# Kernel optimization log

Measured on AMD Instinct MI355X. Metric: run time of the kernel, lower is better.

Reference implementation:

```python
import jax, jax.numpy as jnp
import numpy as np
import math

D_MODEL = 1024
NUM_HEADS = 16
D_HEAD = D_MODEL // NUM_HEADS
BATCH = 2
SEQ = 2048
ROPE_BASE = 10000.0


def get_rotary_embedding(seq_len, d_head):
    # standard RoPE tables: cos/sin of shape [seq_len, d_head]
    inv_freq = 1.0 / (ROPE_BASE ** (jnp.arange(0, d_head, 2, dtype=jnp.float32) / d_head))
    t = jnp.arange(seq_len, dtype=jnp.float32)
    freqs = jnp.outer(t, inv_freq)                      # [S, d_head/2]
    emb = jnp.concatenate([freqs, freqs], axis=-1)      # [S, d_head]
    return jnp.cos(emb), jnp.sin(emb)


def rotate_half(x):
    x1, x2 = jnp.split(x, 2, axis=-1)
    return jnp.concatenate([-x2, x1], axis=-1)


def apply_rotary_pos_emb(x, cos, sin):
    # x: [B, H, S, Dh]; cos/sin: [S, Dh] broadcast over B, H
    return x * cos[None, None, :, :] + rotate_half(x) * sin[None, None, :, :]


def setup_inputs() -> dict:
    key = jax.random.key(0)
    ks = jax.random.split(key, 9)
    s = 1.0 / math.sqrt(D_MODEL)
    inp = {
        "x":  jax.random.normal(ks[0], (BATCH, SEQ, D_MODEL), dtype=jnp.float32),
        "Wq": jax.random.uniform(ks[1], (D_MODEL, D_MODEL), jnp.float32, -s, s),
        "bq": jnp.zeros((D_MODEL,), jnp.float32),
        "Wk": jax.random.uniform(ks[2], (D_MODEL, D_MODEL), jnp.float32, -s, s),
        "bk": jnp.zeros((D_MODEL,), jnp.float32),
        "Wv": jax.random.uniform(ks[3], (D_MODEL, D_MODEL), jnp.float32, -s, s),
        "bv": jnp.zeros((D_MODEL,), jnp.float32),
        "Wo": jax.random.uniform(ks[4], (D_MODEL, D_MODEL), jnp.float32, -s, s),
        "bo": jnp.zeros((D_MODEL,), jnp.float32),
    }
    return inp


def reference(x, Wq, bq, Wk, bk, Wv, bv, Wo, bo) -> jnp.ndarray:
    B, S, _ = x.shape
    H, Dh = NUM_HEADS, D_HEAD

    def proj(W, b):
        y = jnp.einsum('bsd,ed->bse', x, W) + b          # nn.Linear: x @ W^T + b
        return y.reshape(B, S, H, Dh).transpose(0, 2, 1, 3)  # [B,H,S,Dh]

    Q = proj(Wq, bq)
    K = proj(Wk, bk)
    V = proj(Wv, bv)

    cos, sin = get_rotary_embedding(S, Dh)
    Q = apply_rotary_pos_emb(Q, cos, sin)
    K = apply_rotary_pos_emb(K, cos, sin)

    scores = jnp.einsum('bhqd,bhkd->bhqk', Q, K) / math.sqrt(Dh)  # [B,H,S,S]
    causal = jnp.tril(jnp.ones((S, S), dtype=bool))
    scores = jnp.where(causal[None, None, :, :], scores, -jnp.inf)
    attn = jax.nn.softmax(scores, axis=-1)
    # dropout is identity in eval / p=0
    context = jnp.einsum('bhqk,bhkd->bhqd', attn, V)               # [B,H,S,Dh]
    context = context.transpose(0, 2, 1, 3).reshape(B, S, H * Dh)
    return jnp.einsum('bsd,ed->bse', context, Wo) + bo
```

## Files before the change

kernel.cpp:

```cpp
#include <hip/hip_runtime.h>
#include <hip/hip_bf16.h>
#include <math.h>

typedef __attribute__((ext_vector_type(8))) short short8;
typedef __attribute__((ext_vector_type(8))) __bf16 bf16x8;
typedef __attribute__((ext_vector_type(4))) float f32x4;
typedef __attribute__((ext_vector_type(16))) float f32x16;

#define D_MODEL 1024
#define NUM_HEADS 16
#define D_HEAD 64
#define BATCH 2
#define SEQ 2048
#define BH (BATCH * NUM_HEADS)
#define MTOT (BATCH * SEQ)

__device__ inline f32x4 mfma16(short8 a, short8 b, f32x4 c) {
  return __builtin_amdgcn_mfma_f32_16x16x32_bf16(
      __builtin_bit_cast(bf16x8, a), __builtin_bit_cast(bf16x8, b), c, 0, 0, 0);
}

__device__ inline f32x16 mfma32(short8 a, short8 b, f32x16 c) {
  return __builtin_amdgcn_mfma_f32_32x32x16_bf16(
      __builtin_bit_cast(bf16x8, a), __builtin_bit_cast(bf16x8, b), c, 0, 0, 0);
}

__device__ inline unsigned short f2b(float f) {
  __hip_bfloat16 h = __float2bfloat16(f);
  return __builtin_bit_cast(unsigned short, h);
}

__device__ inline unsigned cvt_pk_bf16(float lo, float hi) {
  unsigned r;
  asm("v_cvt_pk_bf16_f32 %0, %1, %2" : "=v"(r) : "v"(lo), "v"(hi));
  return r;
}

__device__ inline float exp2_hw(float x) {
  float r;
  asm("v_exp_f32 %0, %1" : "=v"(r) : "v"(x));
  return r;
}

__device__ inline void permlane32_swap(unsigned& a, unsigned& b) {
  asm("v_permlane32_swap_b32 %0, %1" : "+v"(a), "+v"(b));
}

__device__ __forceinline__ void wait_barrier_vm0() {
  asm volatile("s_waitcnt vmcnt(0)\n\ts_barrier" ::: "memory");
}

#define GLOAD_LDS16(gaddr, laddr)                                              \
  __builtin_amdgcn_global_load_lds(                                            \
      (const __attribute__((address_space(1))) void*)(gaddr),                  \
      (__attribute__((address_space(3))) void*)(laddr), 16, 0, 0)

__global__ void cvt_f32_bf16(const float* __restrict__ in,
                             unsigned short* __restrict__ out, int n) {
  int i = (blockIdx.x * 256 + threadIdx.x) * 4;
  if (i >= n) return;
  float4 v = *(const float4*)(in + i);
  ushort4 o;
  o.x = f2b(v.x); o.y = f2b(v.y); o.z = f2b(v.z); o.w = f2b(v.w);
  *(ushort4*)(out + i) = o;
}

__global__ void cvt4_f32_bf16(const float* __restrict__ w0, const float* __restrict__ w1,
                              const float* __restrict__ w2, const float* __restrict__ w3,
                              unsigned short* __restrict__ o0, unsigned short* __restrict__ o1,
                              unsigned short* __restrict__ o2, unsigned short* __restrict__ o3,
                              int n) {
  const float* in; unsigned short* out;
  switch (blockIdx.y) {
    case 0: in = w0; out = o0; break;
    case 1: in = w1; out = o1; break;
    case 2: in = w2; out = o2; break;
    default: in = w3; out = o3; break;
  }
  int i = (blockIdx.x * 256 + threadIdx.x) * 4;
  if (i >= n) return;
  float4 v = *(const float4*)(in + i);
  ushort4 o;
  o.x = f2b(v.x); o.y = f2b(v.y); o.z = f2b(v.z); o.w = f2b(v.w);
  *(ushort4*)(out + i) = o;
}

__global__ void trig_kernel(float2* __restrict__ tct) {
  int idx = blockIdx.x * 256 + threadIdx.x;
  int i = idx & 31;
  int s = idx >> 5;
  float inv = powf(10000.0f, -(float)i / 32.0f);
  float t = (float)s * inv;
  tct[idx] = make_float2(cosf(t), sinf(t));
}

#define STAGE64(t, bufi)                                                        \
  do {                                                                          \
    const int _k0 = (t) * 64;                                                   \
    const int _gc = ((lane & 7) ^ (lane >> 3)) * 8;                             \
    const int _lc = (lane & 7) * 8;                                             \
    for (int j = 0; j < 4; j++) {                                               \
      const int _r = w * 32 + j * 8 + (lane >> 3);                              \
      GLOAD_LDS16(&A[(size_t)(bm + _r) * D_MODEL + _k0 + _gc], &As[bufi][_r][_lc]); \
      GLOAD_LDS16(&Bp[(size_t)(bn + _r) * D_MODEL + _k0 + _gc], &Bs[bufi][_r][_lc]); \
    }                                                                           \
  } while (0)

#define KLOOP64()                                                               \
  do {                                                                          \
    const int NT = D_MODEL / 64;                                                \
    STAGE64(0, 0);                                                              \
    for (int t = 0; t < NT; ++t) {                                              \
      const int cur = t & 1;                                                    \
      wait_barrier_vm0();                                                       \
      if (t + 1 < NT) STAGE64(t + 1, cur ^ 1);                                  \
      for (int kk = 0; kk < 2; kk++) {                                          \
        short8 af[4], bf4[4];                                                   \
        for (int mi = 0; mi < 4; mi++)                                          \
          af[mi] = *(const short8*)&As[cur][wr + mi * 16 + fr]                  \
                                         [(kk * 32 + fk) ^ ((fr & 7) << 3)];    \
        for (int ni = 0; ni < 4; ni++)                                          \
          bf4[ni] = *(const short8*)&Bs[cur][wc + ni * 16 + fr]                 \
                                          [(kk * 32 + fk) ^ ((fr & 7) << 3)];   \
        __builtin_amdgcn_s_setprio(1);                                          \
        for (int mi = 0; mi < 4; mi++)                                          \
          for (int ni = 0; ni < 4; ni++)                                        \
            acc[mi][ni] = mfma16(af[mi], bf4[ni], acc[mi][ni]);                 \
        __builtin_amdgcn_s_setprio(0);                                          \
      }                                                                         \
    }                                                                           \
  } while (0)

__global__ __launch_bounds__(256) void gemm_qkv(
    const unsigned short* __restrict__ A,
    const unsigned short* __restrict__ Bp,
    const float* __restrict__ bq, const float* __restrict__ bk,
    const float* __restrict__ bv,
    const float2* __restrict__ tct,
    unsigned short* __restrict__ Qb, unsigned short* __restrict__ Kb,
    unsigned short* __restrict__ Vt) {
  __shared__ unsigned short As[2][128][64];
  __shared__ unsigned short Bs[2][128][64];
  const int bm = blockIdx.y * 128;
  const int bn = blockIdx.x * 128;
  const int tid = threadIdx.x;
  const int lane = tid & 63;
  const int w = tid >> 6;
  const int wr = (w >> 1) * 64, wc = (w & 1) * 64;
  const int fr = lane & 15;
  const int g = lane >> 4;
  const int fk = g * 8;

  f32x4 acc[4][4] = {};
  KLOOP64();

  const int type = bn >> 10;
  const int cloc = (bn & 1023) + wc;
  if (type <= 1) {
    const float* bias = (type == 0) ? bq : bk;
    unsigned short* outp = (type == 0) ? Qb : Kb;
    const float SC = (type == 0) ? 0.125f * 1.44269504f : 1.0f;
    const int h = cloc >> 6;
    for (int mi = 0; mi < 4; mi++)
      for (int r = 0; r < 4; r++) {
        int row = bm + wr + mi * 16 + g * 4 + r;
        int b = row >> 11, s = row & (SEQ - 1);
        size_t base = (((size_t)(b * NUM_HEADS + h)) * SEQ + s) * 64;
        for (int ni = 0; ni < 2; ni++) {
          int i = ni * 16 + fr;
          float x0 = acc[mi][ni][r] + bias[cloc + i];
          float x1 = acc[mi][ni + 2][r] + bias[cloc + i + 32];
          float2 cs = tct[s * 32 + i];
          outp[base + i]      = f2b((x0 * cs.x - x1 * cs.y) * SC);
          outp[base + i + 32] = f2b((x1 * cs.x + x0 * cs.y) * SC);
        }
      }
  } else {
    for (int mi = 0; mi < 4; mi++) {
      int row0 = bm + wr + mi * 16 + g * 4;
      int b = row0 >> 11, s0 = row0 & (SEQ - 1);
      for (int ni = 0; ni < 4; ni++) {
        int col = cloc + ni * 16 + fr;
        int h = col >> 6, dh = col & 63;
        float bvv = bv[col];
        uint2 pk = make_uint2(
            cvt_pk_bf16(acc[mi][ni][0] + bvv, acc[mi][ni][1] + bvv),
            cvt_pk_bf16(acc[mi][ni][2] + bvv, acc[mi][ni][3] + bvv));
        *(uint2*)&Vt[(((size_t)(b * NUM_HEADS + h)) * 64 + dh) * SEQ + s0] = pk;
      }
    }
  }
}

__global__ __launch_bounds__(256) void gemm_out(
    const unsigned short* __restrict__ A,
    const unsigned short* __restrict__ Bp,
    const float* __restrict__ bias,
    float* __restrict__ outf) {
  __shared__ unsigned short As[2][128][64];
  __shared__ unsigned short Bs[2][128][64];
  const int bm = blockIdx.y * 128;
  const int bn = blockIdx.x * 128;
  const int tid = threadIdx.x;
  const int lane = tid & 63;
  const int w = tid >> 6;
  const int wr = (w >> 1) * 64, wc = (w & 1) * 64;
  const int fr = lane & 15;
  const int g = lane >> 4;
  const int fk = g * 8;

  f32x4 acc[4][4] = {};
  KLOOP64();

  for (int mi = 0; mi < 4; mi++)
    for (int ni = 0; ni < 4; ni++)
      for (int r = 0; r < 4; r++) {
        int row = bm + wr + mi * 16 + g * 4 + r;
        int col = bn + wc + ni * 16 + fr;
        outf[(size_t)row * D_MODEL + col] = acc[mi][ni][r] + bias[col];
      }
}

__global__ __launch_bounds__(128) void flash_attn(
    const unsigned short* __restrict__ Q,
    const unsigned short* __restrict__ Km,
    const unsigned short* __restrict__ Vt,
    unsigned short* __restrict__ ctx) {
  __shared__ unsigned short Ks[64 * 64];
  __shared__ unsigned short Vs[64 * 64];
  const int bh = blockIdx.x;
  const int qb = 31 - (int)blockIdx.y;
  const int tid = threadIdx.x;
  const int lane = tid & 63;
  const int w = tid >> 6;
  const int q31 = lane & 31;
  const int hi = lane >> 5;

  const unsigned short* Qp = Q + (size_t)bh * SEQ * 64;
  const unsigned short* Kp = Km + (size_t)bh * SEQ * 64;
  const unsigned short* Vp = Vt + (size_t)bh * 64 * SEQ;
  const int b = bh >> 4, h = bh & 15;

  const int qrow0 = qb * 64 + w * 32;
  const int wmax = qrow0 + 31;
  const int q = qrow0 + q31;

  short8 qf[4];
#pragma unroll
  for (int s = 0; s < 4; s++)
    qf[s] = *(const short8*)&Qp[(size_t)q * 64 + s * 16 + hi * 8];

  const int srow = tid >> 1;
  const int sb = (tid & 1) * 4;
  short8 kst[4], vst[4];
#pragma unroll
  for (int j = 0; j < 4; j++) {
    kst[j] = *(const short8*)&Kp[(size_t)srow * 64 + (sb + j) * 8];
    vst[j] = *(const short8*)&Vp[(size_t)srow * SEQ + (sb + j) * 8];
  }

  f32x16 oacc0 = {}, oacc1 = {};
  float lq = 0.f;
  const int NSTEPS = qb + 1;

  for (int step = 0; step < NSTEPS; ++step) {
    const int kbase = step * 64;
#pragma unroll
    for (int j = 0; j < 4; j++) {
      const int off = srow * 64 + (((sb + j) ^ (srow & 7)) * 8);
      *(short8*)&Ks[off] = kst[j];
      *(short8*)&Vs[off] = vst[j];
    }
    __syncthreads();
    if (step + 1 < NSTEPS) {
      const int nk = kbase + 64;
#pragma unroll
      for (int j = 0; j < 4; j++) {
        kst[j] = *(const short8*)&Kp[(size_t)(nk + srow) * 64 + (sb + j) * 8];
        vst[j] = *(const short8*)&Vp[(size_t)srow * SEQ + nk + (sb + j) * 8];
      }
    }

#pragma unroll
    for (int kt = 0; kt < 2; kt++) {
      const int ktb = kbase + kt * 32;
      if (ktb <= wmax) {
        f32x16 sacc = {};
        const int krow = kt * 32 + q31;
        const int kro = krow * 64;
        const int ksw = krow & 7;
#pragma unroll
        for (int s = 0; s < 4; s++) {
          short8 kf = *(const short8*)&Ks[kro + (((s * 2 + hi) ^ ksw) * 8)];
          sacc = mfma32(kf, qf[s], sacc);
        }
        const bool maskT = (ktb + 31 > qrow0);
        float p[16];
        float rs = 0.f;
#pragma unroll
        for (int reg = 0; reg < 16; reg++) {
          float sv = sacc[reg];
          if (maskT) {
            int key = ktb + (reg & 3) + 8 * (reg >> 2) + 4 * hi;
            sv = (key <= q) ? sv : -INFINITY;
          }
          p[reg] = exp2_hw(sv);
          rs += p[reg];
        }
        lq += rs;
        short8 paf[2];
#pragma unroll
        for (int sl = 0; sl < 2; sl++) {
          const int o = sl * 8;
          unsigned a0 = cvt_pk_bf16(p[o + 0], p[o + 1]);
          unsigned b0 = cvt_pk_bf16(p[o + 4], p[o + 5]);
          permlane32_swap(a0, b0);
          unsigned a1 = cvt_pk_bf16(p[o + 2], p[o + 3]);
          unsigned b1 = cvt_pk_bf16(p[o + 6], p[o + 7]);
          permlane32_swap(a1, b1);
          uint4 u = make_uint4(a0, a1, b0, b1);
          paf[sl] = __builtin_bit_cast(short8, u);
        }
#pragma unroll
        for (int dt = 0; dt < 2; dt++) {
          const int vrow = dt * 32 + q31;
          const int vro = vrow * 64;
          const int vsw = vrow & 7;
#pragma unroll
          for (int sl = 0; sl < 2; sl++) {
            short8 vf = *(const short8*)&Vs[vro + (((kt * 4 + sl * 2 + hi) ^ vsw) * 8)];
            if (dt == 0) oacc0 = mfma32(paf[sl], vf, oacc0);
            else         oacc1 = mfma32(paf[sl], vf, oacc1);
          }
        }
      }
    }
    __syncthreads();
  }

  lq += __shfl_xor(lq, 32);
#pragma unroll
  for (int reg = 0; reg < 16; reg++) {
    const int crow = (reg & 3) + 8 * (reg >> 2) + 4 * hi;
    const float linv = 1.f / __shfl(lq, crow);
    const int row = qrow0 + crow;
    size_t base = ((size_t)b * SEQ + row) * D_MODEL + h * 64 + q31;
    ctx[base]      = f2b(oacc0[reg] * linv);
    ctx[base + 32] = f2b(oacc1[reg] * linv);
  }
}

extern "C" void kernel_launch(void* const* d_in, const int* in_sizes, int n_in,
                              void* d_out, int out_size, void* d_ws, size_t ws_size,
                              hipStream_t stream) {
  const float* x  = (const float*)d_in[0];
  const float* Wq = (const float*)d_in[1];
  const float* bq = (const float*)d_in[2];
  const float* Wk = (const float*)d_in[3];
  const float* bk = (const float*)d_in[4];
  const float* Wv = (const float*)d_in[5];
  const float* bv = (const float*)d_in[6];
  const float* Wo = (const float*)d_in[7];
  const float* bo = (const float*)d_in[8];
  float* out = (float*)d_out;

  char* ws = (char*)d_ws;
  size_t off = 0;
  auto alloc = [&](size_t bytes) {
    char* p = ws + off;
    off += (bytes + 255) & ~(size_t)255;
    return p;
  };
  unsigned short* xb   = (unsigned short*)alloc((size_t)MTOT * D_MODEL * 2);
  unsigned short* wqkv = (unsigned short*)alloc((size_t)3 * D_MODEL * D_MODEL * 2);
  unsigned short* wob  = (unsigned short*)alloc((size_t)D_MODEL * D_MODEL * 2);
  unsigned short* Qb   = (unsigned short*)alloc((size_t)BH * SEQ * 64 * 2);
  unsigned short* Kb   = (unsigned short*)alloc((size_t)BH * SEQ * 64 * 2);
  unsigned short* Vt   = (unsigned short*)alloc((size_t)BH * 64 * SEQ * 2);
  unsigned short* ctxb = (unsigned short*)alloc((size_t)MTOT * D_MODEL * 2);
  float2* tct = (float2*)alloc((size_t)SEQ * 32 * 8);

  int nx = MTOT * D_MODEL;
  int nw = D_MODEL * D_MODEL;
  cvt_f32_bf16<<<nx / 1024, 256, 0, stream>>>(x, xb, nx);
  cvt4_f32_bf16<<<dim3(nw / 1024, 4), 256, 0, stream>>>(
      Wq, Wk, Wv, Wo, wqkv, wqkv + nw, wqkv + 2 * (size_t)nw, wob, nw);
  trig_kernel<<<SEQ * 32 / 256, 256, 0, stream>>>(tct);

  gemm_qkv<<<dim3(3 * D_MODEL / 128, MTOT / 128), 256, 0, stream>>>(
      xb, wqkv, bq, bk, bv, tct, Qb, Kb, Vt);

  flash_attn<<<dim3(BH, 32), 128, 0, stream>>>(Qb, Kb, Vt, ctxb);

  gemm_out<<<dim3(D_MODEL / 128, MTOT / 128), 256, 0, stream>>>(ctxb, wob, bo, out);
}
```

Before: 127.9 us.

## Pair complementary causal query tiles per block with 128-key double-buffered LDS

Each flash-attention block now runs 256 threads and handles two 64-row query tiles, j and 31-j, so every block does a balanced amount of causal work. Both tiles share staged K/V tiles of 128 keys, which are double-buffered in LDS so the trailing barrier can be dropped. This aims to cut load imbalance and halve the number of K/V staging rounds per query row. In exchange LDS use rises fourfold, and the tile for j does wasted staging steps past its causal limit.

```diff
diff --git a/kernel.cpp b/kernel.cpp
--- a/kernel.cpp
+++ b/kernel.cpp
@@ -221,18 +221,20 @@
       }
 }
 
-__global__ __launch_bounds__(128) void flash_attn(
+__global__ __launch_bounds__(256) void flash_attn(
     const unsigned short* __restrict__ Q,
     const unsigned short* __restrict__ Km,
     const unsigned short* __restrict__ Vt,
     unsigned short* __restrict__ ctx) {
-  __shared__ unsigned short Ks[64 * 64];
-  __shared__ unsigned short Vs[64 * 64];
+  __shared__ unsigned short Ks[2][128 * 64];
+  __shared__ unsigned short Vs[2][64 * 128];
   const int bh = blockIdx.x;
-  const int qb = 31 - (int)blockIdx.y;
+  const int j = blockIdx.y;
   const int tid = threadIdx.x;
   const int lane = tid & 63;
   const int w = tid >> 6;
+  const int gi = w >> 1;
+  const int wl = w & 1;
   const int q31 = lane & 31;
   const int hi = lane >> 5;
 
@@ -241,101 +243,105 @@
   const unsigned short* Vp = Vt + (size_t)bh * 64 * SEQ;
   const int b = bh >> 4, h = bh & 15;
 
-  const int qrow0 = qb * 64 + w * 32;
+  const int qt64 = gi ? j : (31 - j);
+  const int qrow0 = qt64 * 64 + wl * 32;
   const int wmax = qrow0 + 31;
   const int q = qrow0 + q31;
 
   short8 qf[4];
-#pragma unroll
   for (int s = 0; s < 4; s++)
     qf[s] = *(const short8*)&Qp[(size_t)q * 64 + s * 16 + hi * 8];
 
-  const int srow = tid >> 1;
-  const int sb = (tid & 1) * 4;
+  const int krow_s = tid >> 1;
+  const int ksl0 = (tid & 1) * 4;
+  const int vrow_s = tid >> 2;
+  const int vsl0 = (tid & 3) * 4;
+
   short8 kst[4], vst[4];
 #pragma unroll
-  for (int j = 0; j < 4; j++) {
-    kst[j] = *(const short8*)&Kp[(size_t)srow * 64 + (sb + j) * 8];
-    vst[j] = *(const short8*)&Vp[(size_t)srow * SEQ + (sb + j) * 8];
+  for (int i = 0; i < 4; i++) {
+    kst[i] = *(const short8*)&Kp[(size_t)krow_s * 64 + (ksl0 + i) * 8];
+    vst[i] = *(const short8*)&Vp[(size_t)vrow_s * SEQ + (vsl0 + i) * 8];
   }
 
   f32x16 oacc0 = {}, oacc1 = {};
   float lq = 0.f;
-  const int NSTEPS = qb + 1;
+  const int NSTEPS = (33 - j) >> 1;
 
   for (int step = 0; step < NSTEPS; ++step) {
-    const int kbase = step * 64;
-#pragma unroll
-    for (int j = 0; j < 4; j++) {
-      const int off = srow * 64 + (((sb + j) ^ (srow & 7)) * 8);
-      *(short8*)&Ks[off] = kst[j];
-      *(short8*)&Vs[off] = vst[j];
+    const int kbase = step * 128;
+    const int cur = step & 1;
+#pragma unroll
+    for (int i = 0; i < 4; i++) {
+      *(short8*)&Ks[cur][krow_s * 64 + (((ksl0 + i) ^ (krow_s & 7)) * 8)] = kst[i];
+      *(short8*)&Vs[cur][vrow_s * 128 + (((vsl0 + i) ^ (vrow_s & 15)) * 8)] = vst[i];
     }
     __syncthreads();
     if (step + 1 < NSTEPS) {
-      const int nk = kbase + 64;
-#pragma unroll
-      for (int j = 0; j < 4; j++) {
-        kst[j] = *(const short8*)&Kp[(size_t)(nk + srow) * 64 + (sb + j) * 8];
-        vst[j] = *(const short8*)&Vp[(size_t)srow * SEQ + nk + (sb + j) * 8];
+      const int nk = kbase + 128;
+#pragma unroll
+      for (int i = 0; i < 4; i++) {
+        kst[i] = *(const short8*)&Kp[(size_t)(nk + krow_s) * 64 + (ksl0 + i) * 8];
+        vst[i] = *(const short8*)&Vp[(size_t)vrow_s * SEQ + nk + (vsl0 + i) * 8];
       }
     }
 
-#pragma unroll
-    for (int kt = 0; kt < 2; kt++) {
-      const int ktb = kbase + kt * 32;
-      if (ktb <= wmax) {
-        f32x16 sacc = {};
-        const int krow = kt * 32 + q31;
-        const int kro = krow * 64;
-        const int ksw = krow & 7;
-#pragma unroll
-        for (int s = 0; s < 4; s++) {
-          short8 kf = *(const short8*)&Ks[kro + (((s * 2 + hi) ^ ksw) * 8)];
-          sacc = mfma32(kf, qf[s], sacc);
-        }
-        const bool maskT = (ktb + 31 > qrow0);
-        float p[16];
-        float rs = 0.f;
-#pragma unroll
-        for (int reg = 0; reg < 16; reg++) {
-          float sv = sacc[reg];
-          if (maskT) {
-            int key = ktb + (reg & 3) + 8 * (reg >> 2) + 4 * hi;
-            sv = (key <= q) ? sv : -INFINITY;
+    if (kbase <= wmax) {
+#pragma unroll
+      for (int kt = 0; kt < 4; kt++) {
+        const int ktb = kbase + kt * 32;
+        if (ktb <= wmax) {
+          f32x16 sacc = {};
+          const int krow = kt * 32 + q31;
+          const int kro = krow * 64;
+          const int ksw = krow & 7;
+          for (int s = 0; s < 4; s++) {
+            short8 kf = *(const short8*)&Ks[cur][kro + (((s * 2 + hi) ^ ksw) * 8)];
+            sacc = mfma32(kf, qf[s], sacc);
           }
-          p[reg] = exp2_hw(sv);
-          rs += p[reg];
-        }
-        lq += rs;
-        short8 paf[2];
-#pragma unroll
-        for (int sl = 0; sl < 2; sl++) {
-          const int o = sl * 8;
-          unsigned a0 = cvt_pk_bf16(p[o + 0], p[o + 1]);
-          unsigned b0 = cvt_pk_bf16(p[o + 4], p[o + 5]);
-          permlane32_swap(a0, b0);
-          unsigned a1 = cvt_pk_bf16(p[o + 2], p[o + 3]);
-          unsigned b1 = cvt_pk_bf16(p[o + 6], p[o + 7]);
-          permlane32_swap(a1, b1);
-          uint4 u = make_uint4(a0, a1, b0, b1);
-          paf[sl] = __builtin_bit_cast(short8, u);
-        }
-#pragma unroll
-        for (int dt = 0; dt < 2; dt++) {
-          const int vrow = dt * 32 + q31;
-          const int vro = vrow * 64;
-          const int vsw = vrow & 7;
+          const bool maskT = (ktb + 31 > qrow0);
+          float p[16];
+          float rs = 0.f;
+#pragma unroll
+          for (int reg = 0; reg < 16; reg++) {
+            float sv = sacc[reg];
+            if (maskT) {
+              int key = ktb + (reg & 3) + 8 * (reg >> 2) + 4 * hi;
+              sv = (key <= q) ? sv : -INFINITY;
+            }
+            p[reg] = exp2_hw(sv);
+            rs += p[reg];
+          }
+          lq += rs;
+          short8 paf[2];
 #pragma unroll
           for (int sl = 0; sl < 2; sl++) {
-            short8 vf = *(const short8*)&Vs[vro + (((kt * 4 + sl * 2 + hi) ^ vsw) * 8)];
-            if (dt == 0) oacc0 = mfma32(paf[sl], vf, oacc0);
-            else         oacc1 = mfma32(paf[sl], vf, oacc1);
+            const int o = sl * 8;
+            unsigned a0 = cvt_pk_bf16(p[o + 0], p[o + 1]);
+            unsigned b0 = cvt_pk_bf16(p[o + 4], p[o + 5]);
+            permlane32_swap(a0, b0);
+            unsigned a1 = cvt_pk_bf16(p[o + 2], p[o + 3]);
+            unsigned b1 = cvt_pk_bf16(p[o + 6], p[o + 7]);
+            permlane32_swap(a1, b1);
+            uint4 u = make_uint4(a0, a1, b0, b1);
+            paf[sl] = __builtin_bit_cast(short8, u);
+          }
+#pragma unroll
+          for (int dt = 0; dt < 2; dt++) {
+            const int vrow = dt * 32 + q31;
+            const int vro = vrow * 128;
+            const int vsw = vrow & 15;
+#pragma unroll
+            for (int sl = 0; sl < 2; sl++) {
+              const int vslot = kt * 4 + sl * 2 + hi;
+              short8 vf = *(const short8*)&Vs[cur][vro + ((vslot ^ vsw) * 8)];
+              if (dt == 0) oacc0 = mfma32(paf[sl], vf, oacc0);
+              else         oacc1 = mfma32(paf[sl], vf, oacc1);
+            }
           }
         }
       }
     }
-    __syncthreads();
   }
 
   lq += __shfl_xor(lq, 32);
@@ -390,7 +396,7 @@
   gemm_qkv<<<dim3(3 * D_MODEL / 128, MTOT / 128), 256, 0, stream>>>(
       xb, wqkv, bq, bk, bv, tct, Qb, Kb, Vt);
 
-  flash_attn<<<dim3(BH, 32), 128, 0, stream>>>(Qb, Kb, Vt, ctxb);
+  flash_attn<<<dim3(BH, 16), 256, 0, stream>>>(Qb, Kb, Vt, ctxb);
 
   gemm_out<<<dim3(D_MODEL / 128, MTOT / 128), 256, 0, stream>>>(ctxb, wob, bo, out);
 }
```

New measurement: 122.1 us. 4.5% less time.
